# Optimization experiments

Measured on AMD Instinct MI355X. Metric: run time of the kernel, lower is better.

The kernel has to match this reference:

```python
import jax, jax.numpy as jnp
import numpy as np

HEAD_DIM = 128


def block_causal_mask(cu_seqlens, seq_len, dtype):
    # positions -> which packed document each token belongs to
    positions = jnp.arange(seq_len)
    seq_ids = jnp.searchsorted(cu_seqlens, positions, side='right') - 1
    same_seq = seq_ids[:, None] == seq_ids[None, :]
    causal = positions[None, :] <= positions[:, None]  # key_pos <= query_pos
    neg_inf = jnp.asarray(float('-inf'), dtype)
    return jnp.where(same_seq & causal, jnp.asarray(0.0, dtype), neg_inf)


def setup_inputs() -> dict:
    key = jax.random.key(0)
    kq, kk, kv = jax.random.split(key, 3)
    B, H, S, D = 1, 8, 4096, HEAD_DIM
    q = jax.random.normal(kq, (B, H, S, D), dtype=jnp.float32)
    k = jax.random.normal(kk, (B, H, S, D), dtype=jnp.float32)
    v = jax.random.normal(kv, (B, H, S, D), dtype=jnp.float32)
    # 4 packed documents of length 1024 each; cu_seqlens[-1] == seq_len
    cu_seqlens = jnp.array([0, 1024, 2048, 3072, 4096], dtype=jnp.int32)
    return {"q": q, "k": k, "v": v, "cu_seqlens": cu_seqlens, "max_seqlen": 1024}


def reference(q, k, v, cu_seqlens, max_seqlen):
    seq_len = q.shape[2]
    scale = 1.0 / jnp.sqrt(jnp.asarray(q.shape[-1], q.dtype))
    mask = block_causal_mask(cu_seqlens, seq_len, q.dtype)  # [S, S]
    # scores: [B, H, Sq, Sk]
    scores = jnp.einsum('bhqd,bhkd->bhqk', q, k) * scale + mask
    probs = jax.nn.softmax(scores, axis=-1)
    return jnp.einsum('bhqk,bhkd->bhqd', probs, v)
```

## Files before the change

kernel.cpp:

```cpp
#include <hip/hip_runtime.h>
#include <hip/hip_bf16.h>


#define HD 128
#define BR 64
#define BC 64

typedef __attribute__((ext_vector_type(8))) short short8;
typedef __attribute__((ext_vector_type(4))) float floatx4;

__device__ inline unsigned packbf2(float lo, float hi) {
    __hip_bfloat162 h2 = __float22bfloat162_rn(make_float2(lo, hi));
    return *reinterpret_cast<unsigned*>(&h2);
}
__device__ inline short bfs(float f) {
    __hip_bfloat16 b = __float2bfloat16(f);
    return *reinterpret_cast<short*>(&b);
}

__device__ inline void gll16(const void* g, void* l) {
    __builtin_amdgcn_global_load_lds(
        (const __attribute__((address_space(1))) unsigned int*)g,
        (__attribute__((address_space(3))) unsigned int*)l, 16, 0, 0);
}

__global__ __launch_bounds__(256) void prepack(
    const float* __restrict__ K, const float* __restrict__ V,
    unsigned short* __restrict__ wsK, unsigned short* __restrict__ wsVT,
    int S)
{
    const int tid = threadIdx.x;
    const int nVblk = 8 * (S >> 6);
    const int bid = blockIdx.x;
    if (bid < nVblk) {
        __shared__ __align__(8) unsigned short sV[HD * 68];
        const int ntile = S >> 6;
        const int h = bid / ntile;
        const int t = bid - h * ntile;
        const float* vb = V + ((size_t)h * S + t * 64) * HD;
        {
            const int rp = tid >> 3;
            const int dc = tid & 7;
            const int r0 = rp * 2;
            const int d0 = dc * 16;
            const float* p0 = vb + (size_t)r0 * HD + d0;
            const float* p1 = p0 + HD;
            float4 a0 = *(const float4*)(p0 + 0),  a1 = *(const float4*)(p0 + 4);
            float4 a2 = *(const float4*)(p0 + 8),  a3 = *(const float4*)(p0 + 12);
            float4 b0 = *(const float4*)(p1 + 0),  b1 = *(const float4*)(p1 + 4);
            float4 b2 = *(const float4*)(p1 + 8),  b3 = *(const float4*)(p1 + 12);
            float av[16] = {a0.x,a0.y,a0.z,a0.w, a1.x,a1.y,a1.z,a1.w,
                            a2.x,a2.y,a2.z,a2.w, a3.x,a3.y,a3.z,a3.w};
            float bv[16] = {b0.x,b0.y,b0.z,b0.w, b1.x,b1.y,b1.z,b1.w,
                            b2.x,b2.y,b2.z,b2.w, b3.x,b3.y,b3.z,b3.w};
            #pragma unroll
            for (int i = 0; i < 16; ++i) {
                unsigned pr = packbf2(av[i], bv[i]);
                *(unsigned*)((char*)sV + ((size_t)(d0 + i) * 68 + r0) * 2) = pr;
            }
        }
        __syncthreads();
        const int d  = tid >> 1;
        const int jj = tid & 1;
        char* dstrow = (char*)wsVT + (((size_t)(h * ntile + t) * HD + d) * 128);
        const int dx = (d & 7) << 4;
        const unsigned short* srow = sV + (size_t)d * 68;
        #pragma unroll
        for (int u = 0; u < 4; ++u) {
            const int j  = jj * 4 + u;
            const int k0 = (j >> 2) * 32 + (j & 3) * 4;
            uint2 lo = *(const uint2*)(srow + k0);
            uint2 hi = *(const uint2*)(srow + k0 + 16);
            uint4 w = make_uint4(lo.x, lo.y, hi.x, hi.y);
            *(uint4*)(dstrow + ((j * 16) ^ dx)) = w;
        }
    } else {
        const int cid = (bid - nVblk) * 256 + tid;
        const int row = cid >> 4;
        const int c   = cid & 15;
        const float* src = K + (size_t)row * HD + c * 8;
        float4 f0 = *(const float4*)src;
        float4 f1 = *(const float4*)(src + 4);
        union { uint4 q; unsigned u[4]; } w;
        w.u[0] = packbf2(f0.x, f0.y); w.u[1] = packbf2(f0.z, f0.w);
        w.u[2] = packbf2(f1.x, f1.y); w.u[3] = packbf2(f1.z, f1.w);
        *(uint4*)((char*)wsK + (size_t)row * 256 + ((c * 16) ^ ((row & 7) << 4))) = w.q;
    }
}

__global__ __launch_bounds__(512, 1) void fa_fwd(
    const float* __restrict__ Q,
    const unsigned short* __restrict__ wsK,
    const unsigned short* __restrict__ wsVT,
    const int* __restrict__ cu_seqlens, int n_cu,
    float* __restrict__ O,
    int S)
{
    __shared__ alignas(16) __hip_bfloat16 sK3[3][BC * HD];
    __shared__ alignas(16) unsigned int   sVT3[3][HD * 32];

    const int tid  = threadIdx.x;
    const int wave = tid >> 6;
    const int gp   = wave >> 2;
    const int wsub = wave & 3;
    const int lane = tid & 63;
    const int quad = lane >> 4;
    const int l16  = lane & 15;
    const int kx   = (l16 & 7) << 4;

    const int nqb = S / BR;
    const int h   = blockIdx.x & 7;
    const int g   = (int)(blockIdx.x >> 3);
    int qb;
    if (nqb == 64) {
        if (g < 32) qb = (g >> 4) * 16 + (15 - (g & 15));
        else        qb = 32 + (((g - 32) >> 4) * 16) + (g & 15);
    } else {
        qb = nqb - 1 - g;
    }
    const int q0    = qb * BR;
    const int qw    = q0 + wsub * 16;
    const int qlane = qw + l16;

    int blk_ds = 0;
    for (int i = 0; i < n_cu; ++i) {
        int c = cu_seqlens[i];
        if (c <= q0) blk_ds = c;
    }
    const int k_begin = blk_ds & ~(BC - 1);
    const int ntiles  = (q0 + BR - 1 - k_begin) / BC + 1;

    const char* gkb = (const char*)wsK + (size_t)h * S * 256;
    const char* gvb = (const char*)wsVT + (size_t)h * (S >> 6) * 16384;
    const int wofs = (wave & 3) * 4096;
    const int lo = wofs + lane * 16;
    auto stage = [&](int kt, int buf) {
        if (gp == 0) {
            const char* gk = gkb + (size_t)kt * 256 + lo;
            char* lk = (char*)&sK3[buf][0] + wofs;
            #pragma unroll
            for (int c = 0; c < 4; ++c) gll16(gk + c * 1024, lk + c * 1024);
        } else {
            const char* gv = gvb + (size_t)(kt >> 6) * 16384 + lo;
            char* lv = (char*)&sVT3[buf][0] + wofs;
            #pragma unroll
            for (int c = 0; c < 4; ++c) gll16(gv + c * 1024, lv + c * 1024);
        }
    };

    const size_t hoff = (size_t)h * S * HD;
    const float* Qh = Q + hoff;
    float*       Oh = O + hoff;

    short8 aq[4];
    {
        const float* qp = Qh + (size_t)qlane * HD + quad * 8;
        #pragma unroll
        for (int ks = 0; ks < 4; ++ks) {
            float4 a0 = *(const float4*)(qp + ks * 32);
            float4 a1 = *(const float4*)(qp + ks * 32 + 4);
            short8 a;
            a[0] = bfs(a0.x); a[1] = bfs(a0.y); a[2] = bfs(a0.z); a[3] = bfs(a0.w);
            a[4] = bfs(a1.x); a[5] = bfs(a1.y); a[6] = bfs(a1.z); a[7] = bfs(a1.w);
            aq[ks] = a;
        }
    }

    int ds_lane = 0;
    for (int i = 0; i < n_cu; ++i) {
        int c = cu_seqlens[i];
        if (c <= qlane) ds_lane = c;
    }

    stage(k_begin, 0);
    if (ntiles > 1) stage(k_begin + BC, 1);

    floatx4 oacc[8];
    #pragma unroll
    for (int dt = 0; dt < 8; ++dt) oacc[dt] = (floatx4){0.f, 0.f, 0.f, 0.f};
    float m_r = -1e30f, l_r = 0.f;

    const float sl = 0.08838834764831845f * 1.4426950408889634f;

    int buf = 0;
    for (int it = 0; it < ntiles; ++it) {
        const int kt = k_begin + it * BC;

        if (it + 1 < ntiles) {
            asm volatile("s_waitcnt vmcnt(4)\n\ts_barrier" ::: "memory");
        } else {
            asm volatile("s_waitcnt vmcnt(0)\n\ts_barrier" ::: "memory");
        }

        if (it + 2 < ntiles) {
            int b2 = buf + 2; if (b2 >= 3) b2 -= 3;
            stage(kt + 2 * BC, b2);
        }

        if (kt + gp * 32 <= qw + 15) {
            const char* kbase = (const char*)&sK3[buf][0];
            const char* vbase = (const char*)&sVT3[buf][0];

            floatx4 sc[2];
            __builtin_amdgcn_s_setprio(1);
            #pragma unroll
            for (int ctl = 0; ctl < 2; ++ctl) {
                const int ct = 2 * gp + ctl;
                if (kt + ct * 16 <= qw + 15) {
                    floatx4 c = (floatx4){0.f, 0.f, 0.f, 0.f};
                    #pragma unroll
                    for (int ks = 0; ks < 4; ++ks) {
                        short8 a = *(const short8*)(kbase + (ct * 16 + l16) * 256
                                                    + (((ks * 4 + quad) << 4) ^ kx));
                        c = __builtin_amdgcn_mfma_f32_16x16x32_bf16(a, aq[ks], c, 0, 0, 0);
                    }
                    sc[ctl] = c;
                } else {
                    sc[ctl] = (floatx4){-1e30f, -1e30f, -1e30f, -1e30f};
                }
            }
            __builtin_amdgcn_s_setprio(0);

            #pragma unroll
            for (int ctl = 0; ctl < 2; ++ctl) {
                if (kt + (2 * gp + ctl) * 16 <= qw + 15) {
                    #pragma unroll
                    for (int r = 0; r < 4; ++r) {
                        const int key = kt + (2 * gp + ctl) * 16 + quad * 4 + r;
                        const bool valid = (key <= qlane) && (key >= ds_lane);
                        float s = sc[ctl][r] * sl;
                        sc[ctl][r] = valid ? s : -1e30f;
                    }
                }
            }

            float mx = fmaxf(fmaxf(fmaxf(sc[0][0], sc[0][1]), fmaxf(sc[0][2], sc[0][3])),
                             fmaxf(fmaxf(sc[1][0], sc[1][1]), fmaxf(sc[1][2], sc[1][3])));
            mx = fmaxf(mx, __shfl_xor(mx, 16, 64));
            mx = fmaxf(mx, __shfl_xor(mx, 32, 64));

            if (__any(mx > m_r + 8.f)) {
                const float mnew = fmaxf(m_r, mx);
                const float al   = exp2f(m_r - mnew);
                m_r = mnew;
                l_r *= al;
                #pragma unroll
                for (int dt = 0; dt < 8; ++dt) {
                    #pragma unroll
                    for (int r = 0; r < 4; ++r)
                        oacc[dt][r] *= al;
                }
            }
            const float live = (m_r > -1e29f) ? 1.f : 0.f;

            float ssum = 0.f;
            #pragma unroll
            for (int ctl = 0; ctl < 2; ++ctl) {
                #pragma unroll
                for (int r = 0; r < 4; ++r) {
                    float p = exp2f(sc[ctl][r] - m_r) * live;
                    sc[ctl][r] = p;
                    ssum += p;
                }
            }
            l_r += ssum;

            union { unsigned u[4]; short8 s; } pu;
            pu.u[0] = packbf2(sc[0][0], sc[0][1]);
            pu.u[1] = packbf2(sc[0][2], sc[0][3]);
            pu.u[2] = packbf2(sc[1][0], sc[1][1]);
            pu.u[3] = packbf2(sc[1][2], sc[1][3]);
            __builtin_amdgcn_s_setprio(1);
            #pragma unroll
            for (int dt = 0; dt < 8; ++dt) {
                union { uint4 q; short8 s; } cv;
                cv.q = *(const uint4*)(vbase + (dt * 16 + l16) * 128
                                       + (((gp * 4 + quad) << 4) ^ kx));
                oacc[dt] = __builtin_amdgcn_mfma_f32_16x16x32_bf16(cv.s, pu.s, oacc[dt], 0, 0, 0);
            }
            __builtin_amdgcn_s_setprio(0);
        }

        ++buf; if (buf >= 3) buf = 0;
    }

    l_r += __shfl_xor(l_r, 16, 64);
    l_r += __shfl_xor(l_r, 32, 64);

    __syncthreads();

    float* obuf = (float*)&sK3[0][0];
    float* lbuf = (float*)&sVT3[0][0];
    if (gp == 1) {
        float* ob = obuf + wsub * 2048;
        #pragma unroll
        for (int dt = 0; dt < 8; ++dt) {
            const int sw = (dt ^ (lane & 7)) << 2;
            float4 st;
            st.x = oacc[dt][0]; st.y = oacc[dt][1];
            st.z = oacc[dt][2]; st.w = oacc[dt][3];
            *(float4*)(ob + lane * 32 + sw) = st;
        }
        if (quad == 0) {
            lbuf[wsub * 128 + l16]      = m_r;
            lbuf[wsub * 128 + 64 + l16] = l_r;
        }
    }
    __syncthreads();
    if (gp == 0) {
        const float m2 = lbuf[wsub * 128 + l16];
        const float l2 = lbuf[wsub * 128 + 64 + l16];
        const float M  = fmaxf(m_r, m2);
        const float w1 = exp2f(m_r - M);
        const float w2 = exp2f(m2 - M);
        const float inv = 1.0f / (w1 * l_r + w2 * l2);
        const float* ob = obuf + wsub * 2048;
        float* op = Oh + (size_t)qlane * HD + quad * 4;
        #pragma unroll
        for (int dt = 0; dt < 8; ++dt) {
            const int sw = (dt ^ (lane & 7)) << 2;
            float4 o2 = *(const float4*)(ob + lane * 32 + sw);
            float4 st;
            st.x = (w1 * oacc[dt][0] + w2 * o2.x) * inv;
            st.y = (w1 * oacc[dt][1] + w2 * o2.y) * inv;
            st.z = (w1 * oacc[dt][2] + w2 * o2.z) * inv;
            st.w = (w1 * oacc[dt][3] + w2 * o2.w) * inv;
            *(float4*)(op + dt * 16) = st;
        }
    }
}

extern "C" void kernel_launch(void* const* d_in, const int* in_sizes, int n_in,
                              void* d_out, int out_size, void* d_ws, size_t ws_size,
                              hipStream_t stream) {
    const float* q = (const float*)d_in[0];
    const float* k = (const float*)d_in[1];
    const float* v = (const float*)d_in[2];
    const int* cu = (const int*)d_in[3];
    const int n_cu = in_sizes[3];
    const int H = 8;
    const int S = in_sizes[0] / (H * HD);
    float* out = (float*)d_out;

    const int nqb = S / BR;
    unsigned short* wsK  = (unsigned short*)d_ws;
    unsigned short* wsVT = wsK + (size_t)H * S * HD;

    const int nVblk = H * (S >> 6);
    const int nKblk = (H * S) / 16;
    prepack<<<dim3(nVblk + nKblk), dim3(256), 0, stream>>>(k, v, wsK, wsVT, S);

    dim3 grid(H * nqb);
    dim3 block(512);
    fa_fwd<<<grid, block, 0, stream>>>(q, wsK, wsVT, cu, n_cu, out, S);
}
```

Before: 142.4 us.

## Widen key tile to 128 with double buffering and remap block order

Doubles the key/value tile width so each wave group handles 64 keys per iteration, halving the number of barrier-synchronised iterations. The triple-buffered prefetch with partial waitcnt becomes a double buffer that waits for all loads before each tile. The query-block to workgroup mapping is also changed to interleave blocks across documents. This trades fewer barriers and more work per tile against less prefetch depth, more wasted work on the causal diagonal, and more registers.

```diff
diff --git a/kernel.cpp b/kernel.cpp
--- a/kernel.cpp
+++ b/kernel.cpp
@@ -4,7 +4,7 @@
 
 #define HD 128
 #define BR 64
-#define BC 64
+#define BC 128
 
 typedef __attribute__((ext_vector_type(8))) short short8;
 typedef __attribute__((ext_vector_type(4))) float floatx4;
@@ -96,8 +96,8 @@
     float* __restrict__ O,
     int S)
 {
-    __shared__ alignas(16) __hip_bfloat16 sK3[3][BC * HD];
-    __shared__ alignas(16) unsigned int   sVT3[3][HD * 32];
+    __shared__ alignas(16) __hip_bfloat16 sK2[2][BC * HD];
+    __shared__ alignas(16) unsigned int   sVT2[2][2 * HD * 32];
 
     const int tid  = threadIdx.x;
     const int wave = tid >> 6;
@@ -113,8 +113,7 @@
     const int g   = (int)(blockIdx.x >> 3);
     int qb;
     if (nqb == 64) {
-        if (g < 32) qb = (g >> 4) * 16 + (15 - (g & 15));
-        else        qb = 32 + (((g - 32) >> 4) * 16) + (g & 15);
+        qb = (g & 3) * 16 + (15 - (g >> 2));
     } else {
         qb = nqb - 1 - g;
     }
@@ -132,19 +131,19 @@
 
     const char* gkb = (const char*)wsK + (size_t)h * S * 256;
     const char* gvb = (const char*)wsVT + (size_t)h * (S >> 6) * 16384;
-    const int wofs = (wave & 3) * 4096;
+    const int wofs = (wave & 3) * 8192;
     const int lo = wofs + lane * 16;
     auto stage = [&](int kt, int buf) {
         if (gp == 0) {
             const char* gk = gkb + (size_t)kt * 256 + lo;
-            char* lk = (char*)&sK3[buf][0] + wofs;
-            #pragma unroll
-            for (int c = 0; c < 4; ++c) gll16(gk + c * 1024, lk + c * 1024);
+            char* lk = (char*)&sK2[buf][0] + wofs;
+            #pragma unroll
+            for (int c = 0; c < 8; ++c) gll16(gk + c * 1024, lk + c * 1024);
         } else {
             const char* gv = gvb + (size_t)(kt >> 6) * 16384 + lo;
-            char* lv = (char*)&sVT3[buf][0] + wofs;
-            #pragma unroll
-            for (int c = 0; c < 4; ++c) gll16(gv + c * 1024, lv + c * 1024);
+            char* lv = (char*)&sVT2[buf][0] + wofs;
+            #pragma unroll
+            for (int c = 0; c < 8; ++c) gll16(gv + c * 1024, lv + c * 1024);
         }
     };
 
@@ -173,7 +172,6 @@
     }
 
     stage(k_begin, 0);
-    if (ntiles > 1) stage(k_begin + BC, 1);
 
     floatx4 oacc[8];
     #pragma unroll
@@ -182,36 +180,29 @@
 
     const float sl = 0.08838834764831845f * 1.4426950408889634f;
 
-    int buf = 0;
     for (int it = 0; it < ntiles; ++it) {
-        const int kt = k_begin + it * BC;
-
-        if (it + 1 < ntiles) {
-            asm volatile("s_waitcnt vmcnt(4)\n\ts_barrier" ::: "memory");
-        } else {
-            asm volatile("s_waitcnt vmcnt(0)\n\ts_barrier" ::: "memory");
-        }
-
-        if (it + 2 < ntiles) {
-            int b2 = buf + 2; if (b2 >= 3) b2 -= 3;
-            stage(kt + 2 * BC, b2);
-        }
-
-        if (kt + gp * 32 <= qw + 15) {
-            const char* kbase = (const char*)&sK3[buf][0];
-            const char* vbase = (const char*)&sVT3[buf][0];
-
-            floatx4 sc[2];
+        const int kt  = k_begin + it * BC;
+        const int buf = it & 1;
+
+        asm volatile("s_waitcnt vmcnt(0)\n\ts_barrier" ::: "memory");
+
+        if (it + 1 < ntiles) stage(kt + BC, buf ^ 1);
+
+        if (kt + gp * 64 <= qw + 15) {
+            const char* kbase = (const char*)&sK2[buf][0];
+            const char* vbase = (const char*)&sVT2[buf][0] + gp * 16384;
+
+            floatx4 sc[4];
             __builtin_amdgcn_s_setprio(1);
             #pragma unroll
-            for (int ctl = 0; ctl < 2; ++ctl) {
-                const int ct = 2 * gp + ctl;
-                if (kt + ct * 16 <= qw + 15) {
+            for (int ctl = 0; ctl < 4; ++ctl) {
+                if (kt + gp * 64 + ctl * 16 <= qw + 15) {
                     floatx4 c = (floatx4){0.f, 0.f, 0.f, 0.f};
                     #pragma unroll
                     for (int ks = 0; ks < 4; ++ks) {
-                        short8 a = *(const short8*)(kbase + (ct * 16 + l16) * 256
-                                                    + (((ks * 4 + quad) << 4) ^ kx));
+                        short8 a = *(const short8*)(kbase
+                            + (gp * 64 + ctl * 16 + l16) * 256
+                            + (((ks * 4 + quad) << 4) ^ kx));
                         c = __builtin_amdgcn_mfma_f32_16x16x32_bf16(a, aq[ks], c, 0, 0, 0);
                     }
                     sc[ctl] = c;
@@ -222,11 +213,11 @@
             __builtin_amdgcn_s_setprio(0);
 
             #pragma unroll
-            for (int ctl = 0; ctl < 2; ++ctl) {
-                if (kt + (2 * gp + ctl) * 16 <= qw + 15) {
+            for (int ctl = 0; ctl < 4; ++ctl) {
+                if (kt + gp * 64 + ctl * 16 <= qw + 15) {
                     #pragma unroll
                     for (int r = 0; r < 4; ++r) {
-                        const int key = kt + (2 * gp + ctl) * 16 + quad * 4 + r;
+                        const int key = kt + gp * 64 + ctl * 16 + quad * 4 + r;
                         const bool valid = (key <= qlane) && (key >= ds_lane);
                         float s = sc[ctl][r] * sl;
                         sc[ctl][r] = valid ? s : -1e30f;
@@ -234,8 +225,11 @@
                 }
             }
 
-            float mx = fmaxf(fmaxf(fmaxf(sc[0][0], sc[0][1]), fmaxf(sc[0][2], sc[0][3])),
-                             fmaxf(fmaxf(sc[1][0], sc[1][1]), fmaxf(sc[1][2], sc[1][3])));
+            float mx01 = fmaxf(fmaxf(fmaxf(sc[0][0], sc[0][1]), fmaxf(sc[0][2], sc[0][3])),
+                               fmaxf(fmaxf(sc[1][0], sc[1][1]), fmaxf(sc[1][2], sc[1][3])));
+            float mx23 = fmaxf(fmaxf(fmaxf(sc[2][0], sc[2][1]), fmaxf(sc[2][2], sc[2][3])),
+                               fmaxf(fmaxf(sc[3][0], sc[3][1]), fmaxf(sc[3][2], sc[3][3])));
+            float mx = fmaxf(mx01, mx23);
             mx = fmaxf(mx, __shfl_xor(mx, 16, 64));
             mx = fmaxf(mx, __shfl_xor(mx, 32, 64));
 
@@ -255,7 +249,7 @@
 
             float ssum = 0.f;
             #pragma unroll
-            for (int ctl = 0; ctl < 2; ++ctl) {
+            for (int ctl = 0; ctl < 4; ++ctl) {
                 #pragma unroll
                 for (int r = 0; r < 4; ++r) {
                     float p = exp2f(sc[ctl][r] - m_r) * live;
@@ -265,23 +259,26 @@
             }
             l_r += ssum;
 
-            union { unsigned u[4]; short8 s; } pu;
-            pu.u[0] = packbf2(sc[0][0], sc[0][1]);
-            pu.u[1] = packbf2(sc[0][2], sc[0][3]);
-            pu.u[2] = packbf2(sc[1][0], sc[1][1]);
-            pu.u[3] = packbf2(sc[1][2], sc[1][3]);
             __builtin_amdgcn_s_setprio(1);
             #pragma unroll
-            for (int dt = 0; dt < 8; ++dt) {
-                union { uint4 q; short8 s; } cv;
-                cv.q = *(const uint4*)(vbase + (dt * 16 + l16) * 128
-                                       + (((gp * 4 + quad) << 4) ^ kx));
-                oacc[dt] = __builtin_amdgcn_mfma_f32_16x16x32_bf16(cv.s, pu.s, oacc[dt], 0, 0, 0);
+            for (int ks = 0; ks < 2; ++ks) {
+                if (kt + gp * 64 + ks * 32 <= qw + 15) {
+                    union { unsigned u[4]; short8 s; } pu;
+                    pu.u[0] = packbf2(sc[2*ks][0],   sc[2*ks][1]);
+                    pu.u[1] = packbf2(sc[2*ks][2],   sc[2*ks][3]);
+                    pu.u[2] = packbf2(sc[2*ks+1][0], sc[2*ks+1][1]);
+                    pu.u[3] = packbf2(sc[2*ks+1][2], sc[2*ks+1][3]);
+                    #pragma unroll
+                    for (int dt = 0; dt < 8; ++dt) {
+                        union { uint4 q; short8 s; } cv;
+                        cv.q = *(const uint4*)(vbase + (dt * 16 + l16) * 128
+                                               + (((ks * 4 + quad) << 4) ^ kx));
+                        oacc[dt] = __builtin_amdgcn_mfma_f32_16x16x32_bf16(cv.s, pu.s, oacc[dt], 0, 0, 0);
+                    }
+                }
             }
             __builtin_amdgcn_s_setprio(0);
         }
-
-        ++buf; if (buf >= 3) buf = 0;
     }
 
     l_r += __shfl_xor(l_r, 16, 64);
@@ -289,8 +286,8 @@
 
     __syncthreads();
 
-    float* obuf = (float*)&sK3[0][0];
-    float* lbuf = (float*)&sVT3[0][0];
+    float* obuf = (float*)&sK2[0][0];
+    float* lbuf = (float*)&sVT2[0][0];
     if (gp == 1) {
         float* ob = obuf + wsub * 2048;
         #pragma unroll
```

Measured after the change: 126.5 us. 11.2% less time.
